# Kernel optimization log

Hardware: AMD Instinct MI355X
Metric: run time of the kernel (lower is better)

Reference implementation:

```python
import jax, jax.numpy as jnp
import numpy as np

# MoE config (mirrors init_kwargs)
E = 8        # num_experts
K = 2        # num_experts_per_tok
H = 1024     # hidden_size
F = 2816     # moe_intermediate_size
B, S = 2, 512
NORM_TOPK = True


def setup_inputs() -> dict:
    key = jax.random.key(0)
    ks = jax.random.split(key, 5)
    x = jax.random.normal(ks[0], (B, S, H), dtype=jnp.float32)
    router_w = jax.random.normal(ks[1], (E, H), dtype=jnp.float32) * 0.02   # nn.Linear(H, E).weight
    gate_proj = jax.random.normal(ks[2], (E, H, F), dtype=jnp.float32) * 0.02
    up_proj = jax.random.normal(ks[3], (E, H, F), dtype=jnp.float32) * 0.02
    down_proj = jax.random.normal(ks[4], (E, F, H), dtype=jnp.float32) * 0.02
    return {"x": x, "router_w": router_w, "gate_proj": gate_proj,
            "up_proj": up_proj, "down_proj": down_proj}


def reference(x, router_w, gate_proj, up_proj, down_proj):
    b, s, h = x.shape
    xf = x.reshape(-1, h)                                    # [T, H]
    # Router: softmax over experts, top-k selection mask
    logits = xf @ router_w.T                                 # [T, E]
    probs = jax.nn.softmax(logits, axis=-1)
    topk_p, topk_i = jax.lax.top_k(probs, K)                 # [T, K]
    routing_map = jax.nn.one_hot(topk_i, E, dtype=probs.dtype).sum(axis=1)  # [T, E] 0/1
    if NORM_TOPK:
        probs = probs / topk_p.sum(-1, keepdims=True)
    weight = probs * routing_map                             # [T, E]; zero for unselected experts
    # Per-expert SwiGLU FFN; combine weighted by routing prob.
    # Dense-masked formulation: mathematically identical to the original
    # gather -> per-expert GEMM -> scatter_add, since weight==0 for unrouted pairs.
    g = jnp.einsum('th,ehf->tef', xf, gate_proj)             # [T, E, F]
    u = jnp.einsum('th,ehf->tef', xf, up_proj)               # [T, E, F]
    m = jax.nn.silu(g) * u                                   # [T, E, F]
    out = jnp.einsum('tef,efh,te->th', m, down_proj, weight) # [T, H]
    return out.reshape(b, s, h)
```

## Files before the change

kernel.cpp:

```cpp
#include <hip/hip_runtime.h>

#define HD 1024
#define FD 2816
#define NE 8
#define NT 1024
#define NSLOT (NT * 2)

typedef short short8 __attribute__((ext_vector_type(8)));
typedef unsigned u32x4 __attribute__((ext_vector_type(4)));
typedef unsigned u32x2 __attribute__((ext_vector_type(2)));
typedef float f32x4 __attribute__((ext_vector_type(4)));
typedef float f32x16 __attribute__((ext_vector_type(16)));

typedef __attribute__((address_space(3))) unsigned lds_u32;
typedef __attribute__((address_space(1))) const unsigned glb_u32;

#define WAITV(N) asm volatile("s_waitcnt vmcnt(" #N ") lgkmcnt(0)" ::: "memory")
#define BARRIER() do { __builtin_amdgcn_s_barrier(); __builtin_amdgcn_sched_barrier(0); } while (0)
#define SB() __builtin_amdgcn_sched_barrier(0)

__device__ __forceinline__ void glds16(const void* g, void* l) {
  __builtin_amdgcn_global_load_lds((glb_u32*)g, (lds_u32*)l, 16, 0, 0);
}

__device__ __forceinline__ short f2bf(float f) {
  unsigned u = __builtin_bit_cast(unsigned, f);
  u += 0x7FFFu + ((u >> 16) & 1u);
  return (short)(u >> 16);
}

__device__ __forceinline__ unsigned cvtpk(float lo, float hi) {
  unsigned r;
  asm("v_cvt_pk_bf16_f32 %0, %1, %2" : "=v"(r) : "v"(lo), "v"(hi));
  return r;
}
__device__ __forceinline__ int imin(int a, int b) { return a < b ? a : b; }

__global__ void router_kernel(const float* __restrict__ x,
                              const float* __restrict__ rw,
                              int* __restrict__ counts,
                              int* __restrict__ tok_i,
                              float* __restrict__ tok_w) {
  const int t = blockIdx.x;
  const int lane = threadIdx.x;
  const float* px = x + (size_t)t * HD;
  float acc[NE];
#pragma unroll
  for (int e = 0; e < NE; e++) acc[e] = 0.f;
  for (int h = lane; h < HD; h += 64) {
    float xv = px[h];
#pragma unroll
    for (int e = 0; e < NE; e++) acc[e] += xv * rw[e * HD + h];
  }
#pragma unroll
  for (int e = 0; e < NE; e++) {
#pragma unroll
    for (int off = 32; off > 0; off >>= 1)
      acc[e] += __shfl_xor(acc[e], off, 64);
  }
  if (lane == 0) {
    float mx = acc[0];
#pragma unroll
    for (int e = 1; e < NE; e++) mx = fmaxf(mx, acc[e]);
    float ex[NE];
#pragma unroll
    for (int e = 0; e < NE; e++) ex[e] = __expf(acc[e] - mx);
    int i1 = 0;
#pragma unroll
    for (int e = 1; e < NE; e++) if (ex[e] > ex[i1]) i1 = e;
    int i2 = (i1 == 0) ? 1 : 0;
#pragma unroll
    for (int e = 0; e < NE; e++) if (e != i1 && ex[e] > ex[i2]) i2 = e;
    float inv = 1.f / (ex[i1] + ex[i2]);
    tok_i[t * 2 + 0] = i1; tok_w[t * 2 + 0] = ex[i1] * inv;
    tok_i[t * 2 + 1] = i2; tok_w[t * 2 + 1] = ex[i2] * inv;
    atomicAdd(&counts[i1], 1);
    atomicAdd(&counts[i2], 1);
  }
}

__global__ void scan_kernel(const int* __restrict__ counts,
                            int* __restrict__ bases,
                            int* __restrict__ cursor) {
  if (threadIdx.x == 0) {
    int s = 0;
    for (int e = 0; e < NE; e++) { bases[e] = s; cursor[e] = s; s += counts[e]; }
    bases[NE] = s;
  }
}

__global__ void fill_kernel(const int* __restrict__ tok_i,
                            const float* __restrict__ tok_w,
                            int* __restrict__ cursor,
                            int* __restrict__ slot_token,
                            float* __restrict__ slot_w,
                            int* __restrict__ slot_of) {
  int t = blockIdx.x * 256 + threadIdx.x;
  if (t >= NT) return;
#pragma unroll
  for (int k = 0; k < 2; k++) {
    int e = tok_i[t * 2 + k];
    int pos = atomicAdd(&cursor[e], 1);
    slot_token[pos] = t;
    slot_w[pos] = tok_w[t * 2 + k];
    slot_of[t * 2 + k] = pos;
  }
}

__global__ void gather_kernel(const float* __restrict__ x,
                              const int* __restrict__ slot_token,
                              short* __restrict__ xg) {
  const int slot = blockIdx.x;
  const int tok = slot_token[slot];
  const int t = threadIdx.x;
  f32x4 v = *(const f32x4*)(x + (size_t)tok * HD + t * 4);
  u32x2 s;
  s[0] = cvtpk(v[0], v[1]);
  s[1] = cvtpk(v[2], v[3]);
  *(u32x2*)&xg[(size_t)slot * HD + t * 4] = s;
}


#define GU_STAGEA(S, koff) do {                                    \
    glds16(asrc[0] + (koff), &As[S][wid * 512]);                   \
    glds16(asrc[1] + (koff), &As[S][2048 + wid * 512]);            \
  } while (0)

#define GU_LOADB(G, U, k0) do {                                    \
    _Pragma("unroll")                                              \
    for (int ks = 0; ks < 2; ks++) {                               \
      _Pragma("unroll")                                            \
      for (int j = 0; j < 8; j++) {                                \
        unsigned idx = lidx + (unsigned)((k0) + ks * 16 + j) * FD; \
        G[ks * 8 + j] = Gw[idx];                                   \
        U[ks * 8 + j] = Uw[idx];                                   \
      }                                                            \
    }                                                              \
  } while (0)

#define GU_COMPUTE(Ab, G, U) do {                                             \
    _Pragma("unroll")                                                         \
    for (int ks = 0; ks < 2; ks++) {                                          \
      const int oct = ks * 2 + l5;                                            \
      short8 a0, a1;                                                          \
      { int r = wm * 64 + l31, p = r >> 1;                                    \
        a0 = *(const short8*)((Ab) + p * 64 +                                 \
              ((((r & 1) << 2) | oct) ^ (p & 7)) * 8); }                      \
      { int r = wm * 64 + 32 + l31, p = r >> 1;                               \
        a1 = *(const short8*)((Ab) + p * 64 +                                 \
              ((((r & 1) << 2) | oct) ^ (p & 7)) * 8); }                      \
      u32x4 ug, uu;                                                           \
      _Pragma("unroll")                                                       \
      for (int t2 = 0; t2 < 4; t2++) {                                        \
        ug[t2] = cvtpk(G[ks * 8 + 2 * t2], G[ks * 8 + 2 * t2 + 1]);           \
        uu[t2] = cvtpk(U[ks * 8 + 2 * t2], U[ks * 8 + 2 * t2 + 1]);           \
      }                                                                       \
      short8 bg = __builtin_bit_cast(short8, ug);                             \
      short8 bu = __builtin_bit_cast(short8, uu);                             \
      accG0 = __builtin_amdgcn_mfma_f32_32x32x16_bf16(a0, bg, accG0, 0, 0, 0);\
      accU0 = __builtin_amdgcn_mfma_f32_32x32x16_bf16(a0, bu, accU0, 0, 0, 0);\
      accG1 = __builtin_amdgcn_mfma_f32_32x32x16_bf16(a1, bg, accG1, 0, 0, 0);\
      accU1 = __builtin_amdgcn_mfma_f32_32x32x16_bf16(a1, bu, accU1, 0, 0, 0);\
    }                                                                         \
  } while (0)

#define GU_ITER(S, T) do {                       \
    GU_COMPUTE(&As[S][0], bG##S, bU##S);         \
    BARRIER();                                   \
    GU_STAGEA(S, ((T) + 3) * 32);                \
    SB();                                        \
    GU_LOADB(bG##S, bU##S, ((T) + 3) * 32);      \
    WAITV(63);                                   \
    BARRIER();                                   \
  } while (0)

__global__ __launch_bounds__(256, 2) void gateup_kernel(
    const short* __restrict__ xg, const float* __restrict__ gate_w,
    const float* __restrict__ up_w, const int* __restrict__ bases,
    short* __restrict__ m_out) {
  const int bx = blockIdx.x;
  const int e = bx / 44, nt = bx - e * 44;
  const int b0 = bases[e];
  const int ne = bases[e + 1] - b0;
  const int row0 = blockIdx.y * 128;
  if (row0 >= ne) return;
  const int n0 = nt * 64;

  __shared__ short As[3][4096];

  const int tid = threadIdx.x;
  const int lane = tid & 63, wid = tid >> 6;
  const int l31 = lane & 31, l5 = lane >> 5;
  const int wm = wid >> 1, wn = wid & 1;

  const short* asrc[2];
#pragma unroll
  for (int q = 0; q < 2; q++) {
    int i = q * 256 + tid;
    int p = i >> 3, j = i & 7;
    int v = j ^ (p & 7);
    int r = 2 * p + (v >> 2), c = v & 3;
    int slot = b0 + imin(row0 + r, ne - 1);
    asrc[q] = xg + (size_t)slot * HD + c * 8;
  }

  const float* Gw = gate_w + (size_t)e * HD * FD;
  const float* Uw = up_w + (size_t)e * HD * FD;
  const unsigned lidx = (unsigned)(l5 * 8) * FD + n0 + wn * 32 + l31;

  f32x16 accG0 = (f32x16)0.f, accG1 = (f32x16)0.f;
  f32x16 accU0 = (f32x16)0.f, accU1 = (f32x16)0.f;
  f32x16 bG0, bU0, bG1, bU1, bG2, bU2;

  GU_STAGEA(0, 0);  SB(); GU_LOADB(bG0, bU0, 0);  SB();
  GU_STAGEA(1, 32); SB(); GU_LOADB(bG1, bU1, 32); SB();
  GU_STAGEA(2, 64); SB(); GU_LOADB(bG2, bU2, 64);
  WAITV(63);
  BARRIER();

  for (int t = 0; t < 27; t += 3) {
    GU_ITER(0, t);
    GU_ITER(1, t + 1);
    GU_ITER(2, t + 2);
  }
  GU_ITER(0, 27);
  GU_ITER(1, 28);
  GU_COMPUTE(&As[2][0], bG2, bU2);
  WAITV(34); BARRIER();
  GU_COMPUTE(&As[0][0], bG0, bU0);
  WAITV(0); BARRIER();
  GU_COMPUTE(&As[1][0], bG1, bU1);

#pragma unroll
  for (int q = 0; q < 16; q++) {
    int rb_ = (q & 3) + 8 * (q >> 2) + 4 * l5;
    {
      int r = row0 + wm * 64 + rb_;
      if (r < ne) {
        int slot = b0 + r;
        float g = accG0[q], u = accU0[q];
        float mv = (g / (1.f + __expf(-g))) * u;
        m_out[(size_t)slot * FD + n0 + wn * 32 + l31] = f2bf(mv);
      }
    }
    {
      int r = row0 + wm * 64 + 32 + rb_;
      if (r < ne) {
        int slot = b0 + r;
        float g = accG1[q], u = accU1[q];
        float mv = (g / (1.f + __expf(-g))) * u;
        m_out[(size_t)slot * FD + n0 + wn * 32 + l31] = f2bf(mv);
      }
    }
  }
}


#define DW_STAGEA(S, koff) glds16(asrc + (koff), &As[S][wid * 512])

#define DW_LOADB(B, k0) do {                                       \
    _Pragma("unroll")                                              \
    for (int ks = 0; ks < 2; ks++) {                               \
      _Pragma("unroll")                                            \
      for (int j = 0; j < 8; j++) {                                \
        unsigned idx = lidx + (unsigned)((k0) + ks * 16 + j) * HD; \
        B[ks * 8 + j] = Dw[idx];                                   \
      }                                                            \
    }                                                              \
  } while (0)

#define DW_COMPUTE(Ab, B) do {                                                \
    _Pragma("unroll")                                                         \
    for (int ks = 0; ks < 2; ks++) {                                          \
      const int oct = ks * 2 + l5;                                            \
      int r = wm * 32 + l31, p = r >> 1;                                      \
      short8 a = *(const short8*)((Ab) + p * 64 +                             \
                  ((((r & 1) << 2) | oct) ^ (p & 7)) * 8);                    \
      u32x4 ub;                                                               \
      _Pragma("unroll")                                                       \
      for (int t2 = 0; t2 < 4; t2++)                                          \
        ub[t2] = cvtpk(B[ks * 8 + 2 * t2], B[ks * 8 + 2 * t2 + 1]);           \
      short8 bf = __builtin_bit_cast(short8, ub);                             \
      acc = __builtin_amdgcn_mfma_f32_32x32x16_bf16(a, bf, acc, 0, 0, 0);     \
    }                                                                         \
  } while (0)

#define DW_ITER(S, T) do {                       \
    DW_COMPUTE(&As[S][0], bv##S);                \
    BARRIER();                                   \
    DW_STAGEA(S, ((T) + 3) * 32);                \
    SB();                                        \
    DW_LOADB(bv##S, ((T) + 3) * 32);             \
    WAITV(34);                                   \
    BARRIER();                                   \
  } while (0)

__global__ __launch_bounds__(256, 3) void down_kernel(
    const short* __restrict__ m_in, const float* __restrict__ dw,
    const int* __restrict__ bases, const float* __restrict__ slot_w,
    float* __restrict__ out_slot) {
  const int bx = blockIdx.x;
  const int e = bx >> 4, nt = bx & 15;
  const int b0 = bases[e];
  const int ne = bases[e + 1] - b0;
  const int row0 = blockIdx.y * 64;
  if (row0 >= ne) return;
  const int n0 = nt * 64;

  __shared__ short As[3][2048];

  const int tid = threadIdx.x;
  const int lane = tid & 63, wid = tid >> 6;
  const int l31 = lane & 31, l5 = lane >> 5;
  const int wm = wid >> 1, wn = wid & 1;

  const short* asrc;
  {
    int p = tid >> 3, j = tid & 7;
    int v = j ^ (p & 7);
    int r = 2 * p + (v >> 2), c = v & 3;
    int slot = b0 + imin(row0 + r, ne - 1);
    asrc = m_in + (size_t)slot * FD + c * 8;
  }

  const float* Dw = dw + (size_t)e * FD * HD;
  const unsigned lidx = (unsigned)(l5 * 8) * HD + n0 + wn * 32 + l31;

  f32x16 acc = (f32x16)0.f;
  f32x16 bv0, bv1, bv2;

  DW_STAGEA(0, 0);  SB(); DW_LOADB(bv0, 0);  SB();
  DW_STAGEA(1, 32); SB(); DW_LOADB(bv1, 32); SB();
  DW_STAGEA(2, 64); SB(); DW_LOADB(bv2, 64);
  WAITV(34);
  BARRIER();

  for (int t = 0; t < 84; t += 3) {
    DW_ITER(0, t);
    DW_ITER(1, t + 1);
    DW_ITER(2, t + 2);
  }
  DW_ITER(0, 84);
  DW_COMPUTE(&As[1][0], bv1);
  WAITV(17); BARRIER();
  DW_COMPUTE(&As[2][0], bv2);
  WAITV(0); BARRIER();
  DW_COMPUTE(&As[0][0], bv0);

#pragma unroll
  for (int q = 0; q < 16; q++) {
    int r = row0 + wm * 32 + (q & 3) + 8 * (q >> 2) + 4 * l5;
    if (r < ne) {
      int slot = b0 + r;
      out_slot[(size_t)slot * HD + n0 + wn * 32 + l31] = acc[q] * slot_w[slot];
    }
  }
}

__global__ void combine_kernel(const float* __restrict__ out_slot,
                               const int* __restrict__ slot_of,
                               float* __restrict__ out) {
  const int t = blockIdx.x;
  const int s0 = slot_of[t * 2];
  const int s1 = slot_of[t * 2 + 1];
  const int i = threadIdx.x * 4;
  f32x4 a = *(const f32x4*)(out_slot + (size_t)s0 * HD + i);
  f32x4 b = *(const f32x4*)(out_slot + (size_t)s1 * HD + i);
  f32x4 c = a + b;
  *(f32x4*)(out + (size_t)t * HD + i) = c;
}

extern "C" void kernel_launch(void* const* d_in, const int* in_sizes, int n_in,
                              void* d_out, int out_size, void* d_ws,
                              size_t ws_size, hipStream_t stream) {
  const float* x = (const float*)d_in[0];
  const float* rw = (const float*)d_in[1];
  const float* gw = (const float*)d_in[2];
  const float* uw = (const float*)d_in[3];
  const float* dw = (const float*)d_in[4];
  float* out = (float*)d_out;

  char* ws = (char*)d_ws;
  int* counts = (int*)(ws + 0);
  int* cursor = (int*)(ws + 64);
  int* bases = (int*)(ws + 128);
  int* tok_i = (int*)(ws + 256);
  float* tok_w = (float*)(ws + 8448);
  int* slot_token = (int*)(ws + 16640);
  float* slot_w = (float*)(ws + 24832);
  int* slot_of = (int*)(ws + 33024);
  short* xg = (short*)(ws + 41216);
  short* m_buf = (short*)(ws + 4235520);
  float* out_slot = (float*)(ws + 15769856);

  (void)hipMemsetAsync(counts, 0, 64, stream);
  router_kernel<<<NT, 64, 0, stream>>>(x, rw, counts, tok_i, tok_w);
  scan_kernel<<<1, 64, 0, stream>>>(counts, bases, cursor);
  fill_kernel<<<NT / 256, 256, 0, stream>>>(tok_i, tok_w, cursor, slot_token,
                                            slot_w, slot_of);
  gather_kernel<<<NSLOT, 256, 0, stream>>>(x, slot_token, xg);
  gateup_kernel<<<dim3(352, 16), 256, 0, stream>>>(xg, gw, uw, bases, m_buf);
  down_kernel<<<dim3(128, 32), 256, 0, stream>>>(m_buf, dw, bases, slot_w,
                                                 out_slot);
  combine_kernel<<<NT, 256, 0, stream>>>(out_slot, slot_of, out);
}
```

Before: 203.9 us.

## Prepack fp32 weights to bf16 tiled layout and stage B via LDS

Adds a pack kernel that converts each fp32 weight tensor to bf16 in an MFMA-friendly k-octet layout every call. The GEMMs can then load B tiles straight into LDS with async global_load_lds instead of doing per-element fp32 register loads and conversions. Gate and up become two separate GEMM passes, with a standalone SiLU kernel after them. The combine kernel is removed in favour of atomicAdd scatter into a zeroed output. This trades extra full-weight read/write passes and atomics for a leaner, higher-occupancy inner loop.

Result: slower. 253.2 us (+24.2%).

```diff
diff --git a/kernel.cpp b/kernel.cpp
--- a/kernel.cpp
+++ b/kernel.cpp
@@ -28,7 +28,6 @@
   u += 0x7FFFu + ((u >> 16) & 1u);
   return (short)(u >> 16);
 }
-
 __device__ __forceinline__ unsigned cvtpk(float lo, float hi) {
   unsigned r;
   asm("v_cvt_pk_bf16_f32 %0, %1, %2" : "=v"(r) : "v"(lo), "v"(hi));
@@ -93,8 +92,7 @@
                             const float* __restrict__ tok_w,
                             int* __restrict__ cursor,
                             int* __restrict__ slot_token,
-                            float* __restrict__ slot_w,
-                            int* __restrict__ slot_of) {
+                            float* __restrict__ slot_w) {
   int t = blockIdx.x * 256 + threadIdx.x;
   if (t >= NT) return;
 #pragma unroll
@@ -103,7 +101,6 @@
     int pos = atomicAdd(&cursor[e], 1);
     slot_token[pos] = t;
     slot_w[pos] = tok_w[t * 2 + k];
-    slot_of[t * 2 + k] = pos;
   }
 }
 
@@ -120,64 +117,81 @@
   *(u32x2*)&xg[(size_t)slot * HD + t * 4] = s;
 }
 
-
-#define GU_STAGEA(S, koff) do {                                    \
-    glds16(asrc[0] + (koff), &As[S][wid * 512]);                   \
-    glds16(asrc[1] + (koff), &As[S][2048 + wid * 512]);            \
-  } while (0)
-
-#define GU_LOADB(G, U, k0) do {                                    \
-    _Pragma("unroll")                                              \
-    for (int ks = 0; ks < 2; ks++) {                               \
-      _Pragma("unroll")                                            \
-      for (int j = 0; j < 8; j++) {                                \
-        unsigned idx = lidx + (unsigned)((k0) + ks * 16 + j) * FD; \
-        G[ks * 8 + j] = Gw[idx];                                   \
-        U[ks * 8 + j] = Uw[idx];                                   \
-      }                                                            \
-    }                                                              \
-  } while (0)
-
-#define GU_COMPUTE(Ab, G, U) do {                                             \
+__global__ __launch_bounds__(256) void pack_kernel(
+    const float* __restrict__ W, short* __restrict__ P, int K, int N) {
+  const int f0 = blockIdx.x * 256;
+  const int kt = blockIdx.y;
+  const int e = blockIdx.z;
+  const int KT = K / 32;
+  const int k0 = kt * 32;
+  __shared__ short L[32 * 264];
+  const int tid = threadIdx.x;
+  const int lc = tid & 63, hc = tid >> 6;
+  const float* src = W + (size_t)e * K * N;
+
+#pragma unroll
+  for (int pass = 0; pass < 8; pass++) {
+    int k = pass * 4 + hc;
+    f32x4 v = *(const f32x4*)(src + (size_t)(k0 + k) * N + f0 + lc * 4);
+    u32x2 s;
+    s[0] = cvtpk(v[0], v[1]);
+    s[1] = cvtpk(v[2], v[3]);
+    *(u32x2*)&L[k * 264 + lc * 4] = s;
+  }
+  __syncthreads();
+#pragma unroll
+  for (int pass = 0; pass < 4; pass++) {
+    int f = pass * 64 + lc;
+    int oct = hc;
+    unsigned w[4];
+#pragma unroll
+    for (int i = 0; i < 4; i++) {
+      unsigned lo = (unsigned short)L[(oct * 8 + 2 * i) * 264 + f];
+      unsigned hi = (unsigned short)L[(oct * 8 + 2 * i + 1) * 264 + f];
+      w[i] = lo | (hi << 16);
+    }
+    size_t off = ((size_t)((e * KT + kt) * 4 + oct)) * N * 8 + (size_t)(f0 + f) * 8;
+    *(u32x4*)&P[off] = *(u32x4*)w;
+  }
+}
+
+
+#define G_STAGE(S, T) do {                                           \
+    glds16(asrc0 + (T) * 32, &As[S][wid * 512]);                     \
+    glds16(asrc1 + (T) * 32, &As[S][2048 + wid * 512]);              \
+    glds16(bsrc + (size_t)(T) * 90112, &Bs[S][wid * 512]);           \
+  } while (0)
+
+#define G_COMPUTE(S) do {                                                     \
     _Pragma("unroll")                                                         \
     for (int ks = 0; ks < 2; ks++) {                                          \
       const int oct = ks * 2 + l5;                                            \
-      short8 a0, a1;                                                          \
+      short8 a0, a1, b;                                                       \
       { int r = wm * 64 + l31, p = r >> 1;                                    \
-        a0 = *(const short8*)((Ab) + p * 64 +                                 \
-              ((((r & 1) << 2) | oct) ^ (p & 7)) * 8); }                      \
+        a0 = *(const short8*)&As[S][p * 64 +                                  \
+              ((((r & 1) << 2) | oct) ^ (p & 7)) * 8]; }                      \
       { int r = wm * 64 + 32 + l31, p = r >> 1;                               \
-        a1 = *(const short8*)((Ab) + p * 64 +                                 \
-              ((((r & 1) << 2) | oct) ^ (p & 7)) * 8); }                      \
-      u32x4 ug, uu;                                                           \
-      _Pragma("unroll")                                                       \
-      for (int t2 = 0; t2 < 4; t2++) {                                        \
-        ug[t2] = cvtpk(G[ks * 8 + 2 * t2], G[ks * 8 + 2 * t2 + 1]);           \
-        uu[t2] = cvtpk(U[ks * 8 + 2 * t2], U[ks * 8 + 2 * t2 + 1]);           \
-      }                                                                       \
-      short8 bg = __builtin_bit_cast(short8, ug);                             \
-      short8 bu = __builtin_bit_cast(short8, uu);                             \
-      accG0 = __builtin_amdgcn_mfma_f32_32x32x16_bf16(a0, bg, accG0, 0, 0, 0);\
-      accU0 = __builtin_amdgcn_mfma_f32_32x32x16_bf16(a0, bu, accU0, 0, 0, 0);\
-      accG1 = __builtin_amdgcn_mfma_f32_32x32x16_bf16(a1, bg, accG1, 0, 0, 0);\
-      accU1 = __builtin_amdgcn_mfma_f32_32x32x16_bf16(a1, bu, accU1, 0, 0, 0);\
+        a1 = *(const short8*)&As[S][p * 64 +                                  \
+              ((((r & 1) << 2) | oct) ^ (p & 7)) * 8]; }                      \
+      { int n = wn * 32 + l31, pn = n >> 1;                                   \
+        b = *(const short8*)&Bs[S][pn * 64 +                                  \
+              ((((n & 1) << 2) | oct) ^ (pn & 7)) * 8]; }                     \
+      acc0 = __builtin_amdgcn_mfma_f32_32x32x16_bf16(a0, b, acc0, 0, 0, 0);   \
+      acc1 = __builtin_amdgcn_mfma_f32_32x32x16_bf16(a1, b, acc1, 0, 0, 0);   \
     }                                                                         \
   } while (0)
 
-#define GU_ITER(S, T) do {                       \
-    GU_COMPUTE(&As[S][0], bG##S, bU##S);         \
-    BARRIER();                                   \
-    GU_STAGEA(S, ((T) + 3) * 32);                \
-    SB();                                        \
-    GU_LOADB(bG##S, bU##S, ((T) + 3) * 32);      \
-    WAITV(63);                                   \
-    BARRIER();                                   \
-  } while (0)
-
-__global__ __launch_bounds__(256, 2) void gateup_kernel(
-    const short* __restrict__ xg, const float* __restrict__ gate_w,
-    const float* __restrict__ up_w, const int* __restrict__ bases,
-    short* __restrict__ m_out) {
+#define G_ITER(S, T) do {    \
+    G_COMPUTE(S);            \
+    BARRIER();               \
+    G_STAGE(S, (T) + 3);     \
+    WAITV(6);                \
+    BARRIER();               \
+  } while (0)
+
+__global__ __launch_bounds__(256, 4) void gemm_gu_kernel(
+    const short* __restrict__ xg, const short* __restrict__ P,
+    const int* __restrict__ bases, short* __restrict__ m_out) {
   const int bx = blockIdx.x;
   const int e = bx / 44, nt = bx - e * 44;
   const int b0 = bases[e];
@@ -187,118 +201,113 @@
   const int n0 = nt * 64;
 
   __shared__ short As[3][4096];
+  __shared__ short Bs[3][2048];
 
   const int tid = threadIdx.x;
   const int lane = tid & 63, wid = tid >> 6;
   const int l31 = lane & 31, l5 = lane >> 5;
   const int wm = wid >> 1, wn = wid & 1;
 
-  const short* asrc[2];
-#pragma unroll
-  for (int q = 0; q < 2; q++) {
-    int i = q * 256 + tid;
-    int p = i >> 3, j = i & 7;
-    int v = j ^ (p & 7);
+  const short *asrc0, *asrc1;
+  {
+    int i = tid;
+    int p = i >> 3, j = i & 7, v = j ^ (p & 7);
     int r = 2 * p + (v >> 2), c = v & 3;
-    int slot = b0 + imin(row0 + r, ne - 1);
-    asrc[q] = xg + (size_t)slot * HD + c * 8;
-  }
-
-  const float* Gw = gate_w + (size_t)e * HD * FD;
-  const float* Uw = up_w + (size_t)e * HD * FD;
-  const unsigned lidx = (unsigned)(l5 * 8) * FD + n0 + wn * 32 + l31;
-
-  f32x16 accG0 = (f32x16)0.f, accG1 = (f32x16)0.f;
-  f32x16 accU0 = (f32x16)0.f, accU1 = (f32x16)0.f;
-  f32x16 bG0, bU0, bG1, bU1, bG2, bU2;
-
-  GU_STAGEA(0, 0);  SB(); GU_LOADB(bG0, bU0, 0);  SB();
-  GU_STAGEA(1, 32); SB(); GU_LOADB(bG1, bU1, 32); SB();
-  GU_STAGEA(2, 64); SB(); GU_LOADB(bG2, bU2, 64);
-  WAITV(63);
+    asrc0 = xg + (size_t)(b0 + imin(row0 + r, ne - 1)) * HD + c * 8;
+    i = 256 + tid;
+    p = i >> 3; j = i & 7; v = j ^ (p & 7);
+    r = 2 * p + (v >> 2); c = v & 3;
+    asrc1 = xg + (size_t)(b0 + imin(row0 + r, ne - 1)) * HD + c * 8;
+  }
+  const short* bsrc;
+  {
+    int p = tid >> 3, j = tid & 7, v = j ^ (p & 7);
+    int r = 2 * p + (v >> 2), c = v & 3;
+    bsrc = P + ((size_t)(e * 32 * 4 + c)) * (FD * 8) + (size_t)(n0 + r) * 8;
+  }
+
+  f32x16 acc0 = (f32x16)0.f, acc1 = (f32x16)0.f;
+
+  G_STAGE(0, 0); G_STAGE(1, 1); G_STAGE(2, 2);
+  WAITV(6);
   BARRIER();
 
   for (int t = 0; t < 27; t += 3) {
-    GU_ITER(0, t);
-    GU_ITER(1, t + 1);
-    GU_ITER(2, t + 2);
-  }
-  GU_ITER(0, 27);
-  GU_ITER(1, 28);
-  GU_COMPUTE(&As[2][0], bG2, bU2);
-  WAITV(34); BARRIER();
-  GU_COMPUTE(&As[0][0], bG0, bU0);
+    G_ITER(0, t);
+    G_ITER(1, t + 1);
+    G_ITER(2, t + 2);
+  }
+  G_ITER(0, 27);
+  G_ITER(1, 28);
+  G_COMPUTE(2);
+  WAITV(3); BARRIER();
+  G_COMPUTE(0);
   WAITV(0); BARRIER();
-  GU_COMPUTE(&As[1][0], bG1, bU1);
+  G_COMPUTE(1);
 
 #pragma unroll
   for (int q = 0; q < 16; q++) {
     int rb_ = (q & 3) + 8 * (q >> 2) + 4 * l5;
     {
       int r = row0 + wm * 64 + rb_;
-      if (r < ne) {
-        int slot = b0 + r;
-        float g = accG0[q], u = accU0[q];
-        float mv = (g / (1.f + __expf(-g))) * u;
-        m_out[(size_t)slot * FD + n0 + wn * 32 + l31] = f2bf(mv);
-      }
+      if (r < ne)
+        m_out[(size_t)(b0 + r) * FD + n0 + wn * 32 + l31] = f2bf(acc0[q]);
     }
     {
       int r = row0 + wm * 64 + 32 + rb_;
-      if (r < ne) {
-        int slot = b0 + r;
-        float g = accG1[q], u = accU1[q];
-        float mv = (g / (1.f + __expf(-g))) * u;
-        m_out[(size_t)slot * FD + n0 + wn * 32 + l31] = f2bf(mv);
-      }
+      if (r < ne)
+        m_out[(size_t)(b0 + r) * FD + n0 + wn * 32 + l31] = f2bf(acc1[q]);
     }
   }
 }
 
-
-#define DW_STAGEA(S, koff) glds16(asrc + (koff), &As[S][wid * 512])
-
-#define DW_LOADB(B, k0) do {                                       \
-    _Pragma("unroll")                                              \
-    for (int ks = 0; ks < 2; ks++) {                               \
-      _Pragma("unroll")                                            \
-      for (int j = 0; j < 8; j++) {                                \
-        unsigned idx = lidx + (unsigned)((k0) + ks * 16 + j) * HD; \
-        B[ks * 8 + j] = Dw[idx];                                   \
-      }                                                            \
-    }                                                              \
-  } while (0)
-
-#define DW_COMPUTE(Ab, B) do {                                                \
+__global__ void silu_kernel(short* __restrict__ mg, const short* __restrict__ mu) {
+  size_t id = (size_t)blockIdx.x * 256 + threadIdx.x;
+  short8 g8 = *(const short8*)&mg[id * 8];
+  short8 u8 = *(const short8*)&mu[id * 8];
+  short8 o;
+#pragma unroll
+  for (int j = 0; j < 8; j++) {
+    float g = __builtin_bit_cast(float, (unsigned)((unsigned short)g8[j]) << 16);
+    float u = __builtin_bit_cast(float, (unsigned)((unsigned short)u8[j]) << 16);
+    o[j] = f2bf((g / (1.f + __expf(-g))) * u);
+  }
+  *(short8*)&mg[id * 8] = o;
+}
+
+
+#define D_STAGE(S, T) do {                                           \
+    glds16(asrc + (T) * 32, &As[S][wid * 512]);                      \
+    glds16(bsrc + (size_t)(T) * 32768, &Bs[S][wid * 512]);           \
+  } while (0)
+
+#define D_COMPUTE(S) do {                                                     \
     _Pragma("unroll")                                                         \
     for (int ks = 0; ks < 2; ks++) {                                          \
       const int oct = ks * 2 + l5;                                            \
-      int r = wm * 32 + l31, p = r >> 1;                                      \
-      short8 a = *(const short8*)((Ab) + p * 64 +                             \
-                  ((((r & 1) << 2) | oct) ^ (p & 7)) * 8);                    \
-      u32x4 ub;                                                               \
-      _Pragma("unroll")                                                       \
-      for (int t2 = 0; t2 < 4; t2++)                                          \
-        ub[t2] = cvtpk(B[ks * 8 + 2 * t2], B[ks * 8 + 2 * t2 + 1]);           \
-      short8 bf = __builtin_bit_cast(short8, ub);                             \
-      acc = __builtin_amdgcn_mfma_f32_32x32x16_bf16(a, bf, acc, 0, 0, 0);     \
+      short8 a, b;                                                            \
+      { int r = wm * 32 + l31, p = r >> 1;                                    \
+        a = *(const short8*)&As[S][p * 64 +                                   \
+              ((((r & 1) << 2) | oct) ^ (p & 7)) * 8]; }                      \
+      { int n = wn * 32 + l31, pn = n >> 1;                                   \
+        b = *(const short8*)&Bs[S][pn * 64 +                                  \
+              ((((n & 1) << 2) | oct) ^ (pn & 7)) * 8]; }                     \
+      acc = __builtin_amdgcn_mfma_f32_32x32x16_bf16(a, b, acc, 0, 0, 0);      \
     }                                                                         \
   } while (0)
 
-#define DW_ITER(S, T) do {                       \
-    DW_COMPUTE(&As[S][0], bv##S);                \
-    BARRIER();                                   \
-    DW_STAGEA(S, ((T) + 3) * 32);                \
-    SB();                                        \
-    DW_LOADB(bv##S, ((T) + 3) * 32);             \
-    WAITV(34);                                   \
-    BARRIER();                                   \
-  } while (0)
-
-__global__ __launch_bounds__(256, 3) void down_kernel(
-    const short* __restrict__ m_in, const float* __restrict__ dw,
+#define D_ITER(S, T) do {    \
+    D_COMPUTE(S);            \
+    BARRIER();               \
+    D_STAGE(S, (T) + 3);     \
+    WAITV(4);                \
+    BARRIER();               \
+  } while (0)
+
+__global__ __launch_bounds__(256, 4) void down_kernel(
+    const short* __restrict__ m_in, const short* __restrict__ P,
     const int* __restrict__ bases, const float* __restrict__ slot_w,
-    float* __restrict__ out_slot) {
+    const int* __restrict__ slot_token, float* __restrict__ out) {
   const int bx = blockIdx.x;
   const int e = bx >> 4, nt = bx & 15;
   const int b0 = bases[e];
@@ -308,6 +317,7 @@
   const int n0 = nt * 64;
 
   __shared__ short As[3][2048];
+  __shared__ short Bs[3][2048];
 
   const int tid = threadIdx.x;
   const int lane = tid & 63, wid = tid >> 6;
@@ -316,58 +326,45 @@
 
   const short* asrc;
   {
-    int p = tid >> 3, j = tid & 7;
-    int v = j ^ (p & 7);
+    int p = tid >> 3, j = tid & 7, v = j ^ (p & 7);
     int r = 2 * p + (v >> 2), c = v & 3;
-    int slot = b0 + imin(row0 + r, ne - 1);
-    asrc = m_in + (size_t)slot * FD + c * 8;
-  }
-
-  const float* Dw = dw + (size_t)e * FD * HD;
-  const unsigned lidx = (unsigned)(l5 * 8) * HD + n0 + wn * 32 + l31;
+    asrc = m_in + (size_t)(b0 + imin(row0 + r, ne - 1)) * FD + c * 8;
+  }
+  const short* bsrc;
+  {
+    int p = tid >> 3, j = tid & 7, v = j ^ (p & 7);
+    int r = 2 * p + (v >> 2), c = v & 3;
+    bsrc = P + ((size_t)(e * 88 * 4 + c)) * (HD * 8) + (size_t)(n0 + r) * 8;
+  }
 
   f32x16 acc = (f32x16)0.f;
-  f32x16 bv0, bv1, bv2;
-
-  DW_STAGEA(0, 0);  SB(); DW_LOADB(bv0, 0);  SB();
-  DW_STAGEA(1, 32); SB(); DW_LOADB(bv1, 32); SB();
-  DW_STAGEA(2, 64); SB(); DW_LOADB(bv2, 64);
-  WAITV(34);
+
+  D_STAGE(0, 0); D_STAGE(1, 1); D_STAGE(2, 2);
+  WAITV(4);
   BARRIER();
 
   for (int t = 0; t < 84; t += 3) {
-    DW_ITER(0, t);
-    DW_ITER(1, t + 1);
-    DW_ITER(2, t + 2);
-  }
-  DW_ITER(0, 84);
-  DW_COMPUTE(&As[1][0], bv1);
-  WAITV(17); BARRIER();
-  DW_COMPUTE(&As[2][0], bv2);
+    D_ITER(0, t);
+    D_ITER(1, t + 1);
+    D_ITER(2, t + 2);
+  }
+  D_ITER(0, 84);
+  D_COMPUTE(1);
+  WAITV(2); BARRIER();
+  D_COMPUTE(2);
   WAITV(0); BARRIER();
-  DW_COMPUTE(&As[0][0], bv0);
+  D_COMPUTE(0);
 
 #pragma unroll
   for (int q = 0; q < 16; q++) {
     int r = row0 + wm * 32 + (q & 3) + 8 * (q >> 2) + 4 * l5;
     if (r < ne) {
       int slot = b0 + r;
-      out_slot[(size_t)slot * HD + n0 + wn * 32 + l31] = acc[q] * slot_w[slot];
+      int tok = slot_token[slot];
+      atomicAdd(&out[(size_t)tok * HD + n0 + wn * 32 + l31],
+                acc[q] * slot_w[slot]);
     }
   }
-}
-
-__global__ void combine_kernel(const float* __restrict__ out_slot,
-                               const int* __restrict__ slot_of,
-                               float* __restrict__ out) {
-  const int t = blockIdx.x;
-  const int s0 = slot_of[t * 2];
-  const int s1 = slot_of[t * 2 + 1];
-  const int i = threadIdx.x * 4;
-  f32x4 a = *(const f32x4*)(out_slot + (size_t)s0 * HD + i);
-  f32x4 b = *(const f32x4*)(out_slot + (size_t)s1 * HD + i);
-  f32x4 c = a + b;
-  *(f32x4*)(out + (size_t)t * HD + i) = c;
 }
 
 extern "C" void kernel_launch(void* const* d_in, const int* in_sizes, int n_in,
@@ -388,19 +385,25 @@
   float* tok_w = (float*)(ws + 8448);
   int* slot_token = (int*)(ws + 16640);
   float* slot_w = (float*)(ws + 24832);
-  int* slot_of = (int*)(ws + 33024);
   short* xg = (short*)(ws + 41216);
-  short* m_buf = (short*)(ws + 4235520);
-  float* out_slot = (float*)(ws + 15769856);
+  short* mg = (short*)(ws + 4235520);
+  short* mu = (short*)(ws + 15769856);
+  short* P  = (short*)(ws + 27304192);
 
   (void)hipMemsetAsync(counts, 0, 64, stream);
+  (void)hipMemsetAsync(out, 0, (size_t)out_size * 4, stream);
   router_kernel<<<NT, 64, 0, stream>>>(x, rw, counts, tok_i, tok_w);
   scan_kernel<<<1, 64, 0, stream>>>(counts, bases, cursor);
   fill_kernel<<<NT / 256, 256, 0, stream>>>(tok_i, tok_w, cursor, slot_token,
-                                            slot_w, slot_of);
+                                            slot_w);
   gather_kernel<<<NSLOT, 256, 0, stream>>>(x, slot_token, xg);
-  gateup_kernel<<<dim3(352, 16), 256, 0, stream>>>(xg, gw, uw, bases, m_buf);
-  down_kernel<<<dim3(128, 32), 256, 0, stream>>>(m_buf, dw, bases, slot_w,
-                                                 out_slot);
-  combine_kernel<<<NT, 256, 0, stream>>>(out_slot, slot_of, out);
-}
+
+  pack_kernel<<<dim3(11, 32, NE), 256, 0, stream>>>(gw, P, HD, FD);
+  gemm_gu_kernel<<<dim3(352, 16), 256, 0, stream>>>(xg, P, bases, mg);
+  pack_kernel<<<dim3(11, 32, NE), 256, 0, stream>>>(uw, P, HD, FD);
+  gemm_gu_kernel<<<dim3(352, 16), 256, 0, stream>>>(xg, P, bases, mu);
+  silu_kernel<<<2816, 256, 0, stream>>>(mg, mu);
+  pack_kernel<<<dim3(4, 88, NE), 256, 0, stream>>>(dw, P, FD, HD);
+  down_kernel<<<dim3(128, 32), 256, 0, stream>>>(mg, P, bases, slot_w,
+                                                 slot_token, out);
+}
```
